# Kernel tuning notes

Measured on AMD Instinct MI355X. Metric: run time of the kernel, lower is better.

## Reference

```python
import jax, jax.numpy as jnp
import numpy as np

N_ITER, K, DIM = 2, 16, 64


def setup_inputs() -> dict:
    key = jax.random.key(0)
    ks = jax.random.split(key, 9)
    B, NE, NU, NR = 8192, 200000, 100000, 32
    return {
        "u": jax.random.randint(ks[0], (B,), 0, NU),
        "v": jax.random.randint(ks[1], (B,), 0, NE),
        "adj_ent": jax.random.randint(ks[2], (NE, K), 0, NE),
        "adj_rel": jax.random.randint(ks[3], (NE, K), 0, NR),
        "usr_emb": jax.random.normal(ks[4], (NU, DIM), jnp.float32) * 0.1,
        "rel_emb": jax.random.normal(ks[5], (NR, DIM), jnp.float32) * 0.1,
        "ent_emb": jax.random.normal(ks[6], (NE, DIM), jnp.float32) * 0.1,
        "W": jax.random.normal(ks[7], (DIM, DIM), jnp.float32) / np.float32(np.sqrt(DIM)),
        "b": jnp.zeros((DIM,), jnp.float32),
    }


def reference(u, v, adj_ent, adj_rel, usr_emb, rel_emb, ent_emb, W, b):
    B = u.shape[0]
    user = usr_emb[u]                                  # [B, D]

    # _get_neighbors: multi-hop fixed-fanout expansion
    entities = [v[:, None]]                            # hop 0: [B, 1]
    relations = []
    for h in range(N_ITER):
        entities.append(adj_ent[entities[h]].reshape(B, -1))   # [B, K^(h+1)]
        relations.append(adj_rel[entities[h]].reshape(B, -1))

    ent_vecs = [ent_emb[e] for e in entities]          # [B, K^h, D] gathers
    rel_vecs = [rel_emb[r] for r in relations]

    # _aggregate: attention-weighted neighbor mix + sum-combine linear
    for i in range(N_ITER):
        act = jnp.tanh if i == N_ITER - 1 else jax.nn.sigmoid
        nxt = []
        for hop in range(N_ITER - i):
            self_v = ent_vecs[hop]                              # [B, m, D]
            neigh = ent_vecs[hop + 1].reshape(B, -1, K, DIM)    # [B, m, K, D]
            rel = rel_vecs[hop].reshape(B, -1, K, DIM)          # [B, m, K, D]
            scores = jnp.einsum('bd,bmkd->bmk', user, rel)      # user-relation
            attn = jax.nn.softmax(scores, axis=-1)              # [B, m, K]
            agg = jnp.einsum('bmk,bmkd->bmd', attn, neigh)      # weighted sum
            nxt.append(act((self_v + agg) @ W + b))             # sum aggregator
        ent_vecs = nxt

    item = ent_vecs[0].reshape(B, DIM)
    return jax.nn.sigmoid(jnp.sum(user * item, axis=1))        # [B]
```

## Files before the change

kernel.cpp:

```cpp
#include <hip/hip_runtime.h>

#define KF    16
#define DIM   64
#define BLOCK 256

__device__ __forceinline__ float fsig(float x) {
    return __builtin_amdgcn_rcpf(1.0f + __expf(-x));
}
__device__ __forceinline__ float ftanh(float x) {
    float e = __expf(2.0f * x);
    return 1.0f - 2.0f * __builtin_amdgcn_rcpf(e + 1.0f);
}

__global__ __launch_bounds__(BLOCK) void kgcn_kernel(
    const int* __restrict__ u, const int* __restrict__ v,
    const int* __restrict__ adj_ent, const int* __restrict__ adj_rel,
    const float* __restrict__ usr_emb, const float* __restrict__ rel_emb,
    const float* __restrict__ ent_emb, const float* __restrict__ W,
    const float* __restrict__ bias, float* __restrict__ out, int B)
{
    __shared__ __align__(16) float W_l[DIM * DIM];
    __shared__ float b_l[DIM];
    __shared__ float urs_l[32];
    __shared__ int   e1l[KF];
    __shared__ float at1l[KF];
    __shared__ int   e2l[4][64];
    __shared__ float at2l[4][64];
    __shared__ __align__(16) float xw[4][DIM];
    __shared__ float part0[4][DIM];
    __shared__ float part2[4][DIM];

    const int tid  = threadIdx.x;
    const int lane = tid & 63;
    const int wv   = tid >> 6;
    const int b    = blockIdx.x;

    {
        const float4* W4  = (const float4*)W;
        float4*       Wl4 = (float4*)W_l;
        #pragma unroll
        for (int i = 0; i < 4; ++i) Wl4[tid + i * BLOCK] = W4[tid + i * BLOCK];
        if (tid < DIM) b_l[tid] = bias[tid];
    }

    const int e0 = v[b];
    float user = 0.0f, ent0v = 0.0f;

    if (wv == 0) {
        user  = usr_emb[(size_t)u[b] * DIM + lane];
        ent0v = ent_emb[(size_t)e0 * DIM + lane];
        xw[0][lane] = user;
        const int r = lane & 31, h = lane >> 5;
        float s = 0.0f;
        #pragma unroll
        for (int dd = 0; dd < 32; ++dd) {
            const int d = h * 32 + dd;
            s += xw[0][d] * rel_emb[r * DIM + d];
        }
        s += __shfl_xor(s, 32);
        if (lane < 32) urs_l[lane] = s;
        const int k  = lane & 15;
        const int e1 = adj_ent[e0 * KF + k];
        const int r1 = adj_rel[e0 * KF + k];
        float sc = urs_l[r1];
        float mx = sc;
        mx = fmaxf(mx, __shfl_xor(mx, 1));
        mx = fmaxf(mx, __shfl_xor(mx, 2));
        mx = fmaxf(mx, __shfl_xor(mx, 4));
        mx = fmaxf(mx, __shfl_xor(mx, 8));
        float e  = __expf(sc - mx);
        float sm = e;
        sm += __shfl_xor(sm, 1);
        sm += __shfl_xor(sm, 2);
        sm += __shfl_xor(sm, 4);
        sm += __shfl_xor(sm, 8);
        if (lane < KF) { e1l[lane] = e1; at1l[lane] = e * __builtin_amdgcn_rcpf(sm); }
    }
    __syncthreads();

    {
        const int ml = lane >> 4;
        const int kk = lane & 15;
        const int mm = wv * 4 + ml;
        const int em = e1l[mm];
        const int e2 = adj_ent[em * KF + kk];
        float sc = urs_l[adj_rel[em * KF + kk]];
        float mx = sc;
        mx = fmaxf(mx, __shfl_xor(mx, 1));
        mx = fmaxf(mx, __shfl_xor(mx, 2));
        mx = fmaxf(mx, __shfl_xor(mx, 4));
        mx = fmaxf(mx, __shfl_xor(mx, 8));
        float e  = __expf(sc - mx);
        float sm = e;
        sm += __shfl_xor(sm, 1);
        sm += __shfl_xor(sm, 2);
        sm += __shfl_xor(sm, 4);
        sm += __shfl_xor(sm, 8);
        e2l[wv][lane]  = e2;
        at2l[wv][lane] = e * __builtin_amdgcn_rcpf(sm);
    }

    auto matvec = [&](float x) -> float {
        xw[wv][lane] = x;
        float a0 = b_l[lane], a1 = 0.0f, a2 = 0.0f, a3 = 0.0f;
        #pragma unroll
        for (int d = 0; d < DIM; d += 16) {
            const float4 x0 = *(const float4*)&xw[wv][d +  0];
            const float4 x1 = *(const float4*)&xw[wv][d +  4];
            const float4 x2 = *(const float4*)&xw[wv][d +  8];
            const float4 x3 = *(const float4*)&xw[wv][d + 12];
            a0 = fmaf(x0.x, W_l[(d +  0) * DIM + lane], a0);
            a0 = fmaf(x0.y, W_l[(d +  1) * DIM + lane], a0);
            a0 = fmaf(x0.z, W_l[(d +  2) * DIM + lane], a0);
            a0 = fmaf(x0.w, W_l[(d +  3) * DIM + lane], a0);
            a1 = fmaf(x1.x, W_l[(d +  4) * DIM + lane], a1);
            a1 = fmaf(x1.y, W_l[(d +  5) * DIM + lane], a1);
            a1 = fmaf(x1.z, W_l[(d +  6) * DIM + lane], a1);
            a1 = fmaf(x1.w, W_l[(d +  7) * DIM + lane], a1);
            a2 = fmaf(x2.x, W_l[(d +  8) * DIM + lane], a2);
            a2 = fmaf(x2.y, W_l[(d +  9) * DIM + lane], a2);
            a2 = fmaf(x2.z, W_l[(d + 10) * DIM + lane], a2);
            a2 = fmaf(x2.w, W_l[(d + 11) * DIM + lane], a2);
            a3 = fmaf(x3.x, W_l[(d + 12) * DIM + lane], a3);
            a3 = fmaf(x3.y, W_l[(d + 13) * DIM + lane], a3);
            a3 = fmaf(x3.z, W_l[(d + 14) * DIM + lane], a3);
            a3 = fmaf(x3.w, W_l[(d + 15) * DIM + lane], a3);
        }
        return (a0 + a1) + (a2 + a3);
    };

    float agg0p = 0.0f, agg2p = 0.0f;
    #pragma unroll 1
    for (int q = 0; q < 4; ++q) {
        const int m = wv * 4 + q;
        float rows[KF + 1];
        #pragma unroll
        for (int k = 0; k < KF; ++k) {
            const int e = __builtin_amdgcn_readfirstlane(e2l[wv][q * 16 + k]);
            rows[k] = ent_emb[(size_t)e * DIM + lane];
        }
        const int es = __builtin_amdgcn_readfirstlane(e1l[m]);
        rows[KF] = ent_emb[(size_t)es * DIM + lane];

        float g0 = 0.0f, g1 = 0.0f, g2 = 0.0f, g3 = 0.0f;
        #pragma unroll
        for (int k = 0; k < KF; k += 4) {
            g0 = fmaf(at2l[wv][q * 16 + k + 0], rows[k + 0], g0);
            g1 = fmaf(at2l[wv][q * 16 + k + 1], rows[k + 1], g1);
            g2 = fmaf(at2l[wv][q * 16 + k + 2], rows[k + 2], g2);
            g3 = fmaf(at2l[wv][q * 16 + k + 3], rows[k + 3], g3);
        }
        const float selfv = rows[KF];
        const float x     = selfv + ((g0 + g1) + (g2 + g3));
        const float h1m   = fsig(matvec(x));
        const float a1m   = at1l[m];
        agg2p = fmaf(a1m, h1m, agg2p);
        agg0p = fmaf(a1m, selfv, agg0p);
    }

    part0[wv][lane] = agg0p;
    part2[wv][lane] = agg2p;
    __syncthreads();

    if (wv == 0) {
        const float agg0 = (part0[0][lane] + part0[1][lane]) + (part0[2][lane] + part0[3][lane]);
        const float agg2 = (part2[0][lane] + part2[1][lane]) + (part2[2][lane] + part2[3][lane]);
        const float h0   = fsig(matvec(ent0v + agg0));
        const float item = ftanh(matvec(h0 + agg2));
        float p = user * item;
        p += __shfl_xor(p, 1);
        p += __shfl_xor(p, 2);
        p += __shfl_xor(p, 4);
        p += __shfl_xor(p, 8);
        p += __shfl_xor(p, 16);
        p += __shfl_xor(p, 32);
        if (lane == 0) out[b] = fsig(p);
    }
}

extern "C" void kernel_launch(void* const* d_in, const int* in_sizes, int n_in,
                              void* d_out, int out_size, void* d_ws, size_t ws_size,
                              hipStream_t stream) {
    const int*   u       = (const int*)d_in[0];
    const int*   v       = (const int*)d_in[1];
    const int*   adj_ent = (const int*)d_in[2];
    const int*   adj_rel = (const int*)d_in[3];
    const float* usr_emb = (const float*)d_in[4];
    const float* rel_emb = (const float*)d_in[5];
    const float* ent_emb = (const float*)d_in[6];
    const float* W       = (const float*)d_in[7];
    const float* bias    = (const float*)d_in[8];
    float* out = (float*)d_out;

    const int B = in_sizes[0];
    kgcn_kernel<<<B, BLOCK, 0, stream>>>(u, v, adj_ent, adj_rel,
                                         usr_emb, rel_emb, ent_emb,
                                         W, bias, out, B);
}
```

Measured before the change: 211.1 us.

## Replace scalar LDS matvecs with bf16 MFMA over batched hop-1 rows

Removes the 16KB shared-memory copy of W and the per-wave scalar 64x64 matvecs. Each wave instead holds a 16-column slice of W as bf16 MFMA B-fragments in registers. The 16 hop-1 inputs are staged in LDS as bf16 and multiplied in one 16x16x32 MFMA pair per wave, and the two final matvecs reuse the same MFMA path with a single valid row. This lowers LDS footprint and FMA work and may raise occupancy. The cost is bf16 rounding of activations and weights, plus several extra block-wide barriers.

```diff
diff --git a/kernel.cpp b/kernel.cpp
--- a/kernel.cpp
+++ b/kernel.cpp
@@ -4,12 +4,20 @@
 #define DIM   64
 #define BLOCK 256
 
+typedef __attribute__((ext_vector_type(8))) short bs8;
+typedef __attribute__((ext_vector_type(4))) float f32x4;
+
 __device__ __forceinline__ float fsig(float x) {
     return __builtin_amdgcn_rcpf(1.0f + __expf(-x));
 }
 __device__ __forceinline__ float ftanh(float x) {
     float e = __expf(2.0f * x);
     return 1.0f - 2.0f * __builtin_amdgcn_rcpf(e + 1.0f);
+}
+__device__ __forceinline__ ushort f2bf(float x) {
+    uint u = __builtin_bit_cast(uint, x);
+    u += 0x7fffu + ((u >> 16) & 1u);
+    return (ushort)(u >> 16);
 }
 
 __global__ __launch_bounds__(BLOCK) void kgcn_kernel(
@@ -19,29 +27,34 @@
     const float* __restrict__ ent_emb, const float* __restrict__ W,
     const float* __restrict__ bias, float* __restrict__ out, int B)
 {
-    __shared__ __align__(16) float W_l[DIM * DIM];
     __shared__ float b_l[DIM];
     __shared__ float urs_l[32];
     __shared__ int   e1l[KF];
     __shared__ float at1l[KF];
     __shared__ int   e2l[4][64];
     __shared__ float at2l[4][64];
-    __shared__ __align__(16) float xw[4][DIM];
+    __shared__ __align__(16) ushort Xl[16][72];
     __shared__ float part0[4][DIM];
-    __shared__ float part2[4][DIM];
+    __shared__ float xbuf[DIM];
+    __shared__ float agg2s[DIM];
+    __shared__ float psum[4];
 
     const int tid  = threadIdx.x;
     const int lane = tid & 63;
     const int wv   = tid >> 6;
     const int b    = blockIdx.x;
-
-    {
-        const float4* W4  = (const float4*)W;
-        float4*       Wl4 = (float4*)W_l;
-        #pragma unroll
-        for (int i = 0; i < 4; ++i) Wl4[tid + i * BLOCK] = W4[tid + i * BLOCK];
-        if (tid < DIM) b_l[tid] = bias[tid];
-    }
+    const int lr   = lane & 15;
+    const int lg   = lane >> 4;
+    const int col  = wv * 16 + lr;
+
+    bs8 wf0, wf1;
+    #pragma unroll
+    for (int i = 0; i < 8; ++i) {
+        const int k = lg * 8 + i;
+        wf0[i] = (short)f2bf(W[k * DIM + col]);
+        wf1[i] = (short)f2bf(W[(k + 32) * DIM + col]);
+    }
+    if (tid < DIM) b_l[tid] = bias[tid];
 
     const int e0 = v[b];
     float user = 0.0f, ent0v = 0.0f;
@@ -49,13 +62,13 @@
     if (wv == 0) {
         user  = usr_emb[(size_t)u[b] * DIM + lane];
         ent0v = ent_emb[(size_t)e0 * DIM + lane];
-        xw[0][lane] = user;
+        xbuf[lane] = user;
         const int r = lane & 31, h = lane >> 5;
         float s = 0.0f;
         #pragma unroll
         for (int dd = 0; dd < 32; ++dd) {
             const int d = h * 32 + dd;
-            s += xw[0][d] * rel_emb[r * DIM + d];
+            s += xbuf[d] * rel_emb[r * DIM + d];
         }
         s += __shfl_xor(s, 32);
         if (lane < 32) urs_l[lane] = s;
@@ -79,12 +92,10 @@
     __syncthreads();
 
     {
-        const int ml = lane >> 4;
-        const int kk = lane & 15;
-        const int mm = wv * 4 + ml;
+        const int mm = wv * 4 + lg;
         const int em = e1l[mm];
-        const int e2 = adj_ent[em * KF + kk];
-        float sc = urs_l[adj_rel[em * KF + kk]];
+        const int e2 = adj_ent[em * KF + lr];
+        float sc = urs_l[adj_rel[em * KF + lr]];
         float mx = sc;
         mx = fmaxf(mx, __shfl_xor(mx, 1));
         mx = fmaxf(mx, __shfl_xor(mx, 2));
@@ -100,36 +111,7 @@
         at2l[wv][lane] = e * __builtin_amdgcn_rcpf(sm);
     }
 
-    auto matvec = [&](float x) -> float {
-        xw[wv][lane] = x;
-        float a0 = b_l[lane], a1 = 0.0f, a2 = 0.0f, a3 = 0.0f;
-        #pragma unroll
-        for (int d = 0; d < DIM; d += 16) {
-            const float4 x0 = *(const float4*)&xw[wv][d +  0];
-            const float4 x1 = *(const float4*)&xw[wv][d +  4];
-            const float4 x2 = *(const float4*)&xw[wv][d +  8];
-            const float4 x3 = *(const float4*)&xw[wv][d + 12];
-            a0 = fmaf(x0.x, W_l[(d +  0) * DIM + lane], a0);
-            a0 = fmaf(x0.y, W_l[(d +  1) * DIM + lane], a0);
-            a0 = fmaf(x0.z, W_l[(d +  2) * DIM + lane], a0);
-            a0 = fmaf(x0.w, W_l[(d +  3) * DIM + lane], a0);
-            a1 = fmaf(x1.x, W_l[(d +  4) * DIM + lane], a1);
-            a1 = fmaf(x1.y, W_l[(d +  5) * DIM + lane], a1);
-            a1 = fmaf(x1.z, W_l[(d +  6) * DIM + lane], a1);
-            a1 = fmaf(x1.w, W_l[(d +  7) * DIM + lane], a1);
-            a2 = fmaf(x2.x, W_l[(d +  8) * DIM + lane], a2);
-            a2 = fmaf(x2.y, W_l[(d +  9) * DIM + lane], a2);
-            a2 = fmaf(x2.z, W_l[(d + 10) * DIM + lane], a2);
-            a2 = fmaf(x2.w, W_l[(d + 11) * DIM + lane], a2);
-            a3 = fmaf(x3.x, W_l[(d + 12) * DIM + lane], a3);
-            a3 = fmaf(x3.y, W_l[(d + 13) * DIM + lane], a3);
-            a3 = fmaf(x3.z, W_l[(d + 14) * DIM + lane], a3);
-            a3 = fmaf(x3.w, W_l[(d + 15) * DIM + lane], a3);
-        }
-        return (a0 + a1) + (a2 + a3);
-    };
-
-    float agg0p = 0.0f, agg2p = 0.0f;
+    float agg0p = 0.0f;
     #pragma unroll 1
     for (int q = 0; q < 4; ++q) {
         const int m = wv * 4 + q;
@@ -152,30 +134,71 @@
         }
         const float selfv = rows[KF];
         const float x     = selfv + ((g0 + g1) + (g2 + g3));
-        const float h1m   = fsig(matvec(x));
-        const float a1m   = at1l[m];
-        agg2p = fmaf(a1m, h1m, agg2p);
-        agg0p = fmaf(a1m, selfv, agg0p);
-    }
-
+        agg0p = fmaf(at1l[m], selfv, agg0p);
+        Xl[m][lane] = f2bf(x);
+    }
     part0[wv][lane] = agg0p;
-    part2[wv][lane] = agg2p;
+    __syncthreads();
+
+    const float bj = b_l[col];
+    f32x4 c; c[0] = bj; c[1] = bj; c[2] = bj; c[3] = bj;
+    {
+        const ushort* arow = &Xl[lr][lg * 8];
+        bs8 a0 = *(const bs8*)arow;
+        bs8 a1 = *(const bs8*)(arow + 32);
+        c = __builtin_amdgcn_mfma_f32_16x16x32_bf16(a0, wf0, c, 0, 0, 0);
+        c = __builtin_amdgcn_mfma_f32_16x16x32_bf16(a1, wf1, c, 0, 0, 0);
+    }
+    {
+        float p = 0.0f;
+        #pragma unroll
+        for (int r = 0; r < 4; ++r) p = fmaf(at1l[lg * 4 + r], fsig(c[r]), p);
+        p += __shfl_xor(p, 16);
+        p += __shfl_xor(p, 32);
+        if (lane < 16) agg2s[col] = p;
+    }
     __syncthreads();
 
     if (wv == 0) {
         const float agg0 = (part0[0][lane] + part0[1][lane]) + (part0[2][lane] + part0[3][lane]);
-        const float agg2 = (part2[0][lane] + part2[1][lane]) + (part2[2][lane] + part2[3][lane]);
-        const float h0   = fsig(matvec(ent0v + agg0));
-        const float item = ftanh(matvec(h0 + agg2));
-        float p = user * item;
-        p += __shfl_xor(p, 1);
-        p += __shfl_xor(p, 2);
-        p += __shfl_xor(p, 4);
-        p += __shfl_xor(p, 8);
-        p += __shfl_xor(p, 16);
-        p += __shfl_xor(p, 32);
-        if (lane == 0) out[b] = fsig(p);
-    }
+        Xl[0][lane] = f2bf(ent0v + agg0);
+    }
+    __syncthreads();
+
+    c[0] = bj; c[1] = bj; c[2] = bj; c[3] = bj;
+    {
+        const ushort* arow = &Xl[lr][lg * 8];
+        bs8 a0 = *(const bs8*)arow;
+        bs8 a1 = *(const bs8*)(arow + 32);
+        c = __builtin_amdgcn_mfma_f32_16x16x32_bf16(a0, wf0, c, 0, 0, 0);
+        c = __builtin_amdgcn_mfma_f32_16x16x32_bf16(a1, wf1, c, 0, 0, 0);
+    }
+    __syncthreads();
+    if (lane < 16) {
+        const float h0 = fsig(c[0]);
+        Xl[0][col] = f2bf(h0 + agg2s[col]);
+    }
+    __syncthreads();
+
+    c[0] = bj; c[1] = bj; c[2] = bj; c[3] = bj;
+    {
+        const ushort* arow = &Xl[lr][lg * 8];
+        bs8 a0 = *(const bs8*)arow;
+        bs8 a1 = *(const bs8*)(arow + 32);
+        c = __builtin_amdgcn_mfma_f32_16x16x32_bf16(a0, wf0, c, 0, 0, 0);
+        c = __builtin_amdgcn_mfma_f32_16x16x32_bf16(a1, wf1, c, 0, 0, 0);
+    }
+    float pv = 0.0f;
+    if (lane < 16) pv = xbuf[col] * ftanh(c[0]);
+    pv += __shfl_xor(pv, 1);
+    pv += __shfl_xor(pv, 2);
+    pv += __shfl_xor(pv, 4);
+    pv += __shfl_xor(pv, 8);
+    pv += __shfl_xor(pv, 16);
+    pv += __shfl_xor(pv, 32);
+    if (lane == 0) psum[wv] = pv;
+    __syncthreads();
+    if (tid == 0) out[b] = fsig((psum[0] + psum[1]) + (psum[2] + psum[3]));
 }
 
 extern "C" void kernel_launch(void* const* d_in, const int* in_sizes, int n_in,
```

Result: faster. 203.0 us (-3.8%).
